# Performance work log

Hardware: AMD Instinct MI355X
Metric: run time of the kernel (lower is better)

## Reference

```python
import jax, jax.numpy as jnp
import numpy as np

S1, S2 = 1024, 1024
DA, DV, DOUT = 2, 64, 1
K1, K2 = 32, 32


def _gelu(x):
    # torch nn.GELU() default is the exact erf-based gelu
    return jax.nn.gelu(x, approximate=False)


def _flayer(Rr, Ri, w, x):
    f = jnp.fft.rfftn(x, axes=(0, 1))[:K1, :K2]            # [K1,K2,DV] complex
    Rf = jnp.einsum('abc,abcd->abd', f, Rr + 1j * Ri)       # [K1,K2,DV] complex
    kernelpart = jnp.fft.irfftn(Rf, s=(S1, S2), axes=(0, 1))  # [S1,S2,DV] real
    return _gelu(kernelpart + x @ w)


def setup_inputs() -> dict:
    key = jax.random.key(0)
    ks = jax.random.split(key, 20)
    d = {}
    d['input'] = jax.random.normal(ks[0], (S1, S2, DA), dtype=jnp.float32)
    d['Wsh'] = jax.random.normal(ks[1], (DA, DV), dtype=jnp.float32) * (1.0 / np.sqrt(DA))
    d['bsh'] = jax.random.normal(ks[2], (DV,), dtype=jnp.float32) * 0.02
    for i, base in zip(range(1, 5), range(3, 15, 3)):
        d[f'Rr{i}'] = jax.random.normal(ks[base], (K1, K2, DV, DV), dtype=jnp.float32) * (1.0 / DV)
        d[f'Ri{i}'] = jax.random.normal(ks[base + 1], (K1, K2, DV, DV), dtype=jnp.float32) * (1.0 / DV)
        d[f'w{i}'] = jax.random.normal(ks[base + 2], (DV, DV), dtype=jnp.float32) * (1.0 / np.sqrt(DV))
    d['Wp'] = jax.random.normal(ks[15], (DV, DOUT), dtype=jnp.float32) * (1.0 / np.sqrt(DV))
    d['bp'] = jax.random.normal(ks[16], (DOUT,), dtype=jnp.float32) * 0.02
    return d


def reference(input, Wsh, bsh, Rr1, Ri1, w1, Rr2, Ri2, w2,
              Rr3, Ri3, w3, Rr4, Ri4, w4, Wp, bp):
    vt = _gelu(input @ Wsh + bsh)          # Shallow: Linear + GELU
    vt = _flayer(Rr1, Ri1, w1, vt)
    vt = _flayer(Rr2, Ri2, w2, vt)
    vt = _flayer(Rr3, Ri3, w3, vt)
    vt = _flayer(Rr4, Ri4, w4, vt)
    u = (vt @ Wp + bp)[:, :, 0]            # Project, take channel 0 -> [S1,S2]
    return u
```

## Files before the change

kernel.cpp:

```cpp
#include <hip/hip_runtime.h>
#include <math.h>

#define MASKN 1023

typedef unsigned short ushort_t;
typedef __attribute__((ext_vector_type(8))) short short8;
typedef __attribute__((ext_vector_type(4))) float floatx4;
typedef __attribute__((ext_vector_type(4))) unsigned short us4v;

__device__ __forceinline__ float gelu_f(float x) {
    float x2 = x * x;
    float inner = fmaf(0.044715f * x, x2, x);
    float t = exp2f(inner * -2.302089214f);
    return x * __builtin_amdgcn_rcpf(1.0f + t);
}

__device__ __forceinline__ float bf2f(ushort_t h) {
    return __uint_as_float(((unsigned int)h) << 16);
}
__device__ __forceinline__ ushort_t f2bf(float f) {
    unsigned int u = __float_as_uint(f);
    u += 0x7FFFu + ((u >> 16) & 1u);
    return (ushort_t)(u >> 16);
}
struct us4 { ushort_t x, y, z, w; };

__device__ __forceinline__ unsigned int pk2bf(float lo, float hi) {
    unsigned int r;
    asm("v_cvt_pk_bf16_f32 %0, %1, %2" : "=v"(r) : "v"(lo), "v"(hi));
    return r;
}

__device__ __forceinline__ void st4(ushort_t* p, float4 v) {
    uint2 w;
    w.x = pk2bf(v.x, v.y);
    w.y = pk2bf(v.z, v.w);
    *(uint2*)p = w;
}

__device__ __forceinline__ void async16(ushort_t* l, const ushort_t* g) {
    __builtin_amdgcn_global_load_lds(
        (const __attribute__((address_space(1))) void*)g,
        (__attribute__((address_space(3))) void*)l, 16, 0, 0);
}

__global__ void k_fill_tw(float* __restrict__ ct, float* __restrict__ st) {
    int j = blockIdx.x * 256 + threadIdx.x;
    float ang = (float)j * (6.283185307179586f / 1024.0f);
    float s, c;
    sincosf(ang, &s, &c);
    ct[j] = c; st[j] = s;
}

__global__ void k_fill_T1(ushort_t* __restrict__ T1h, ushort_t* __restrict__ T1l) {
    int idx = blockIdx.x * 256 + threadIdx.x;
    int k2p = idx >> 10, y = idx & 1023;
    int k2 = k2p >> 1;
    float ang = (float)((k2 * y) & MASKN) * (6.283185307179586f / 1024.0f);
    float s, c;
    sincosf(ang, &s, &c);
    float v = (k2p & 1) ? -s : c;
    ushort_t h = f2bf(v);
    T1h[idx] = h;
    T1l[idx] = f2bf(v - bf2f(h));
}

__global__ void k_fill_T2(ushort_t* __restrict__ T2h, ushort_t* __restrict__ T2l) {
    int idx = blockIdx.x * 256 + threadIdx.x;
    int n2 = idx >> 6, kk = idx & 63;
    int k2 = kk >> 1;
    float ang = (float)((k2 * n2) & MASKN) * (6.283185307179586f / 1024.0f);
    float s, c;
    sincosf(ang, &s, &c);
    float v = (kk & 1) ? -s : c;
    ushort_t h = f2bf(v);
    T2h[idx] = h;
    T2l[idx] = f2bf(v - bf2f(h));
}

__global__ void k_fill_wT(const float* __restrict__ w1, const float* __restrict__ w2,
        const float* __restrict__ w3, const float* __restrict__ w4,
        ushort_t* __restrict__ wTh, ushort_t* __restrict__ wTl) {
    int l = blockIdx.y;
    int i = blockIdx.x * 256 + threadIdx.x;
    int d = i >> 6, c = i & 63;
    const float* w = (l == 0) ? w1 : (l == 1) ? w2 : (l == 2) ? w3 : w4;
    float v = w[c * 64 + d];
    ushort_t h = f2bf(v);
    wTh[l * 4096 + i] = h;
    wTl[l * 4096 + i] = f2bf(v - bf2f(h));
}

__global__ __launch_bounds__(256) void k_shallow(const float* __restrict__ in,
        const float* __restrict__ Wsh, const float* __restrict__ bsh,
        ushort_t* __restrict__ vt) {
    int tid = blockIdx.x * 256 + threadIdx.x;
    int p = tid >> 4, c0 = (tid & 15) << 2;
    float a0 = in[p * 2], a1 = in[p * 2 + 1];
    float4 w0 = *(const float4*)&Wsh[c0];
    float4 w1 = *(const float4*)&Wsh[64 + c0];
    float4 b  = *(const float4*)&bsh[c0];
    float4 r;
    r.x = gelu_f(fmaf(a0, w0.x, fmaf(a1, w1.x, b.x)));
    r.y = gelu_f(fmaf(a0, w0.y, fmaf(a1, w1.y, b.y)));
    r.z = gelu_f(fmaf(a0, w0.z, fmaf(a1, w1.z, b.z)));
    r.w = gelu_f(fmaf(a0, w0.w, fmaf(a1, w1.w, b.w)));
    st4(&vt[(size_t)p * 64 + c0], r);
}

#define VS1 72
__global__ __launch_bounds__(256, 3) void k_f1(const ushort_t* __restrict__ vt,
        const ushort_t* __restrict__ T1h, const ushort_t* __restrict__ T1l,
        float* __restrict__ gT) {
    __shared__ __align__(16) ushort_t t1s[2][8192];
    __shared__ __align__(16) ushort_t vs[2][64 * VS1];
    int t = threadIdx.x;
    int x0 = blockIdx.x * 2;
    int wv = t >> 6, lane = t & 63;
    int lm = lane & 15, quad = lane >> 4;
    int lrow = t & 63, cq = (t >> 6) * 16;
    const ushort_t* vrow0 = vt + (size_t)x0 * 65536;
    const ushort_t* vrow1 = vrow0 + 65536;

    floatx4 acc[2][4];
    #pragma unroll
    for (int xi = 0; xi < 2; ++xi)
        #pragma unroll
        for (int nt = 0; nt < 4; ++nt) acc[xi][nt] = (floatx4)(0.f);

    uint4 pf[2][2][2];
    #pragma unroll
    for (int i = 0; i < 4; ++i) {
        int j = (wv * 4 + i) * 64 + lane;
        int jj = j & 511;
        int r = jj >> 3, du = jj & 7, su = du ^ (r & 7);
        const ushort_t* src = ((j < 512) ? T1h : T1l) + (size_t)r * 1024 + su * 8;
        async16(&t1s[0][(wv * 4 + i) * 512], src);
    }
    __builtin_amdgcn_sched_barrier(0);
    {
        const ushort_t* s00 = vrow0 + (size_t)lrow * 64 + cq;
        pf[0][0][0] = *(const uint4*)(s00);
        pf[0][0][1] = *(const uint4*)(s00 + 8);
        const ushort_t* s01 = vrow1 + (size_t)lrow * 64 + cq;
        pf[0][1][0] = *(const uint4*)(s01);
        pf[0][1][1] = *(const uint4*)(s01 + 8);
        const ushort_t* s10 = vrow0 + (size_t)(64 + lrow) * 64 + cq;
        pf[1][0][0] = *(const uint4*)(s10);
        pf[1][0][1] = *(const uint4*)(s10 + 8);
        const ushort_t* s11 = vrow1 + (size_t)(64 + lrow) * 64 + cq;
        pf[1][1][0] = *(const uint4*)(s11);
        pf[1][1][1] = *(const uint4*)(s11 + 8);
    }
    __builtin_amdgcn_sched_barrier(0);

    for (int hc = 0; hc < 16; ++hc) {
        int b = hc & 1;
        #pragma unroll
        for (int xi = 0; xi < 2; ++xi)
            #pragma unroll
            for (int i = 0; i < 2; ++i) {
                union { uint4 u; ushort_t e[8]; } uv;
                uv.u = pf[b][xi][i];
                #pragma unroll
                for (int j = 0; j < 8; ++j)
                    vs[xi][(cq + i * 8 + j) * VS1 + lrow] = uv.e[j];
            }
        __builtin_amdgcn_sched_barrier(0);
        if (hc < 15) asm volatile("s_waitcnt vmcnt(4)" ::: "memory");
        else         asm volatile("s_waitcnt vmcnt(0)" ::: "memory");
        __builtin_amdgcn_sched_barrier(0);
        __builtin_amdgcn_s_barrier();
        if (hc < 15) {
            #pragma unroll
            for (int i = 0; i < 4; ++i) {
                int j = (wv * 4 + i) * 64 + lane;
                int jj = j & 511;
                int r = jj >> 3, du = jj & 7, su = du ^ (r & 7);
                const ushort_t* src = ((j < 512) ? T1h : T1l)
                                      + (size_t)r * 1024 + (hc + 1) * 64 + su * 8;
                async16(&t1s[b ^ 1][(wv * 4 + i) * 512], src);
            }
        }
        if (hc < 14) {
            const ushort_t* s0 = vrow0 + (size_t)((hc + 2) * 64 + lrow) * 64 + cq;
            pf[b][0][0] = *(const uint4*)(s0);
            pf[b][0][1] = *(const uint4*)(s0 + 8);
            const ushort_t* s1 = vrow1 + (size_t)((hc + 2) * 64 + lrow) * 64 + cq;
            pf[b][1][0] = *(const uint4*)(s1);
            pf[b][1][1] = *(const uint4*)(s1 + 8);
        }
        __builtin_amdgcn_sched_barrier(0);

        #pragma unroll
        for (int ys = 0; ys < 2; ++ys) {
            short8 af0 = *(const short8*)&vs[0][(wv * 16 + lm) * VS1 + ys * 32 + quad * 8];
            short8 af1 = *(const short8*)&vs[1][(wv * 16 + lm) * VS1 + ys * 32 + quad * 8];
            #pragma unroll
            for (int nt = 0; nt < 4; ++nt) {
                int sl = (((ys * 4 + quad) ^ (lm & 7)) * 8);
                short8 bh = *(const short8*)&t1s[b][(nt * 16 + lm) * 64 + sl];
                short8 bl = *(const short8*)&t1s[b][4096 + (nt * 16 + lm) * 64 + sl];
                acc[0][nt] = __builtin_amdgcn_mfma_f32_16x16x32_bf16(af0, bh, acc[0][nt], 0, 0, 0);
                acc[0][nt] = __builtin_amdgcn_mfma_f32_16x16x32_bf16(af0, bl, acc[0][nt], 0, 0, 0);
                acc[1][nt] = __builtin_amdgcn_mfma_f32_16x16x32_bf16(af1, bh, acc[1][nt], 0, 0, 0);
                acc[1][nt] = __builtin_amdgcn_mfma_f32_16x16x32_bf16(af1, bl, acc[1][nt], 0, 0, 0);
            }
        }
    }
    #pragma unroll
    for (int xi = 0; xi < 2; ++xi) {
        float* grow = gT + (size_t)(x0 + xi) * 4096;
        #pragma unroll
        for (int nt = 0; nt < 4; ++nt)
            #pragma unroll
            for (int r = 0; r < 4; ++r)
                grow[(wv * 16 + quad * 4 + r) * 64 + nt * 16 + lm] = acc[xi][nt][r];
    }
}

__global__ __launch_bounds__(256) void k_f2(const float* __restrict__ gT,
        const float* __restrict__ ct, const float* __restrict__ st,
        float* __restrict__ fpr, float* __restrict__ fpi) {
    int t = threadIdx.x;
    int cx = blockIdx.x;
    int cg = blockIdx.y;
    int k10 = blockIdx.z * 8;
    int l = t & 63;
    int q = t >> 6;
    int c = cg * 4 + q;
    int e = l & 1;
    int k2 = l >> 1;
    float acc[8];
    #pragma unroll
    for (int i = 0; i < 8; ++i) acc[i] = 0.f;
    for (int xi = 0; xi < 128; ++xi) {
        int x = cx * 128 + xi;
        float v = gT[(size_t)x * 4096 + c * 64 + l];
        float p = __shfl_xor(v, 1);
        float gr = e ? p : v;
        float gi = e ? v : p;
        float u  = e ? gi : gr;
        float w2 = e ? -gr : gi;
        float cb = ct[x], sb = st[x];
        int ph = (x * k10) & MASKN;
        float cr = ct[ph], sr = st[ph];
        #pragma unroll
        for (int j = 0; j < 8; ++j) {
            acc[j] = fmaf(u, cr, fmaf(w2, sr, acc[j]));
            float nc = fmaf(cr, cb, -sr * sb);
            float ns = fmaf(sr, cb, cr * sb);
            cr = nc; sr = ns;
        }
    }
    float* dst = e ? fpi : fpr;
    #pragma unroll
    for (int j = 0; j < 8; ++j)
        dst[(size_t)cx * 65536 + ((k10 + j) * 32 + k2) * 64 + c] = acc[j];
}

__global__ __launch_bounds__(64) void k_mix(const float* __restrict__ fpr, const float* __restrict__ fpi,
        const float* __restrict__ Rr, const float* __restrict__ Ri,
        float* __restrict__ Rfr, float* __restrict__ Rfi) {
    __shared__ float fr[64], fi[64];
    int m = blockIdx.x;
    int d = threadIdx.x;
    float sr = 0.f, si = 0.f;
    #pragma unroll
    for (int ch = 0; ch < 8; ++ch) {
        sr += fpr[(size_t)ch * 65536 + m * 64 + d];
        si += fpi[(size_t)ch * 65536 + m * 64 + d];
    }
    fr[d] = sr; fi[d] = si;
    __syncthreads();
    const float* Rrb = Rr + (size_t)m * 4096;
    const float* Rib = Ri + (size_t)m * 4096;
    float ar = 0.f, ai = 0.f;
    for (int c = 0; c < 64; ++c) {
        float rr = Rrb[c * 64 + d], ri = Rib[c * 64 + d];
        ar = fmaf(fr[c], rr, fmaf(-fi[c], ri, ar));
        ai = fmaf(fr[c], ri, fmaf(fi[c], rr, ai));
    }
    Rfr[m * 64 + d] = ar;
    Rfi[m * 64 + d] = ai;
}

__global__ __launch_bounds__(256) void k_i1(const float* __restrict__ Rfr, const float* __restrict__ Rfi,
        const float* __restrict__ ctg, const float* __restrict__ stg,
        ushort_t* __restrict__ Bhl) {
    __shared__ float ct[1024], st[1024];
    int t = threadIdx.x;
    #pragma unroll
    for (int i = 0; i < 4; ++i) { int j = t + 256 * i; ct[j] = ctg[j]; st[j] = stg[j]; }
    __syncthreads();
    int n1 = blockIdx.x;
    int d = t & 63;
    int k20 = (t >> 6) * 8;
    float br[8], bi[8];
    #pragma unroll
    for (int j = 0; j < 8; ++j) { br[j] = 0.f; bi[j] = 0.f; }
    int idx = 0;
    for (int k1 = 0; k1 < 32; ++k1) {
        float cc = ct[idx], ss = st[idx];
        idx = (idx + n1) & MASKN;
        #pragma unroll
        for (int j = 0; j < 8; ++j) {
            float rr = Rfr[(k1 * 32 + k20 + j) * 64 + d];
            float ri = Rfi[(k1 * 32 + k20 + j) * 64 + d];
            br[j] = fmaf(rr, cc, fmaf(-ri, ss, br[j]));
            bi[j] = fmaf(rr, ss, fmaf(ri, cc, bi[j]));
        }
    }
    union { uint4 u[2]; ushort_t e[16]; } hh, ll;
    #pragma unroll
    for (int j = 0; j < 8; ++j) {
        int k2 = k20 + j;
        float sc = (k2 == 0 ? 1.0f : 2.0f) * 9.5367431640625e-7f;
        float vr = br[j] * sc, vi = bi[j] * sc;
        ushort_t hr = f2bf(vr), hi2 = f2bf(vi);
        hh.e[2 * j] = hr;          hh.e[2 * j + 1] = hi2;
        ll.e[2 * j] = f2bf(vr - bf2f(hr));
        ll.e[2 * j + 1] = f2bf(vi - bf2f(hi2));
    }
    size_t base = (size_t)n1 * 8192 + d * 64 + 2 * k20;
    *(uint4*)(Bhl + base) = hh.u[0];
    *(uint4*)(Bhl + base + 8) = hh.u[1];
    *(uint4*)(Bhl + 4096 + base) = ll.u[0];
    *(uint4*)(Bhl + 4096 + base + 8) = ll.u[1];
}

__global__ __launch_bounds__(256, 2) void k_i2f(ushort_t* __restrict__ vt,
        ushort_t* Bhl,
        const ushort_t* __restrict__ T2h, const ushort_t* __restrict__ T2l,
        const ushort_t* __restrict__ wTh, const ushort_t* __restrict__ wTl,
        const ushort_t* __restrict__ T1h, const ushort_t* __restrict__ T1l,
        float* gT) {
    __shared__ __align__(16) ushort_t ab[16384];
    __shared__ __align__(16) ushort_t t1s[8192];
    __shared__ __align__(16) ushort_t trans[64 * VS1];
    int t = threadIdx.x;
    int wv = t >> 6, lane = t & 63;
    int lm = lane & 15, quad = lane >> 4;
    int n1 = blockIdx.x;
    const ushort_t* Bhr = Bhl + (size_t)n1 * 8192;
    const ushort_t* Blr = Bhr + 4096;

    {
        const ushort_t* s = (wv == 0) ? Bhr : (wv == 1) ? Blr : (wv == 2) ? wTh : wTl;
        #pragma unroll
        for (int i = 0; i < 8; ++i) {
            int j = i * 64 + lane;
            int r = j >> 3, u = (j & 7) ^ (r & 7);
            async16(&ab[wv * 4096 + i * 512], s + r * 64 + u * 8);
        }
    }

    int n2b = wv * 16 + lm;
    const ushort_t* t2hp = T2h + n2b * 64 + quad * 8;
    const ushort_t* t2lp = T2l + n2b * 64 + quad * 8;
    const ushort_t* vrd  = vt + ((size_t)n1 * 1024 + n2b) * 64 + quad * 8;
    ushort_t*       vst  = vt + ((size_t)n1 * 1024 + n2b) * 64;

    short8 th[2][2], tl[2][2], vv[2][2];
    #pragma unroll
    for (int ks = 0; ks < 2; ++ks) {
        th[0][ks] = *(const short8*)(t2hp + ks * 32);
        tl[0][ks] = *(const short8*)(t2lp + ks * 32);
        vv[0][ks] = *(const short8*)(vrd + ks * 32);
    }
    floatx4 facc[4];
    #pragma unroll
    for (int nt = 0; nt < 4; ++nt) facc[nt] = (floatx4)(0.f);
    __syncthreads();

    int r7 = lm & 7;
    #pragma unroll
    for (int c = 0; c < 16; ++c) {
        #pragma unroll
        for (int i = 0; i < 4; ++i) {
            int j = (wv * 4 + i) * 64 + lane;
            int jj = j & 511;
            int rr_ = jj >> 3, du = jj & 7, su = du ^ (rr_ & 7);
            const ushort_t* src = ((j < 512) ? T1h : T1l)
                                  + (size_t)rr_ * 1024 + c * 64 + su * 8;
            async16(&t1s[(wv * 4 + i) * 512], src);
        }
        __builtin_amdgcn_sched_barrier(0);
        if (c < 15) {
            #pragma unroll
            for (int ks = 0; ks < 2; ++ks) {
                th[(c + 1) & 1][ks] = *(const short8*)(t2hp + (c + 1) * 4096 + ks * 32);
                tl[(c + 1) & 1][ks] = *(const short8*)(t2lp + (c + 1) * 4096 + ks * 32);
                vv[(c + 1) & 1][ks] = *(const short8*)(vrd + (size_t)(c + 1) * 4096 + ks * 32);
            }
        }
        __builtin_amdgcn_sched_barrier(0);

        floatx4 acc[4];
        #pragma unroll
        for (int mt = 0; mt < 4; ++mt) acc[mt] = (floatx4)(0.f);
        __builtin_amdgcn_s_setprio(1);
        #pragma unroll
        for (int ks = 0; ks < 2; ++ks) {
            int sl = ((ks * 4 + quad) ^ r7) * 8;
            #pragma unroll
            for (int mt = 0; mt < 4; ++mt) {
                int ro = (mt * 16 + lm) * 64 + sl;
                short8 ah = *(const short8*)&ab[ro];
                short8 al = *(const short8*)&ab[4096 + ro];
                short8 wh = *(const short8*)&ab[8192 + ro];
                short8 wl = *(const short8*)&ab[12288 + ro];
                acc[mt] = __builtin_amdgcn_mfma_f32_16x16x32_bf16(ah, th[c & 1][ks], acc[mt], 0, 0, 0);
                acc[mt] = __builtin_amdgcn_mfma_f32_16x16x32_bf16(al, th[c & 1][ks], acc[mt], 0, 0, 0);
                acc[mt] = __builtin_amdgcn_mfma_f32_16x16x32_bf16(ah, tl[c & 1][ks], acc[mt], 0, 0, 0);
                acc[mt] = __builtin_amdgcn_mfma_f32_16x16x32_bf16(wh, vv[c & 1][ks], acc[mt], 0, 0, 0);
                acc[mt] = __builtin_amdgcn_mfma_f32_16x16x32_bf16(wl, vv[c & 1][ks], acc[mt], 0, 0, 0);
            }
        }
        __builtin_amdgcn_s_setprio(0);

        uint2 w[4];
        #pragma unroll
        for (int mt = 0; mt < 4; ++mt) {
            w[mt].x = pk2bf(gelu_f(acc[mt][0]), gelu_f(acc[mt][1]));
            w[mt].y = pk2bf(gelu_f(acc[mt][2]), gelu_f(acc[mt][3]));
            *(uint2*)(vst + (size_t)c * 4096 + mt * 16 + quad * 4) = w[mt];
        }
        #pragma unroll
        for (int mt = 0; mt < 4; ++mt) {
            int chb = mt * 16 + quad * 4;
            trans[(chb + 0) * VS1 + n2b] = (ushort_t)(w[mt].x & 0xffffu);
            trans[(chb + 1) * VS1 + n2b] = (ushort_t)(w[mt].x >> 16);
            trans[(chb + 2) * VS1 + n2b] = (ushort_t)(w[mt].y & 0xffffu);
            trans[(chb + 3) * VS1 + n2b] = (ushort_t)(w[mt].y >> 16);
        }
        __builtin_amdgcn_sched_barrier(0);
        asm volatile("s_waitcnt lgkmcnt(0)" ::: "memory");
        if (c < 15) asm volatile("s_waitcnt vmcnt(10)" ::: "memory");
        else        asm volatile("s_waitcnt vmcnt(4)" ::: "memory");
        __builtin_amdgcn_sched_barrier(0);
        __builtin_amdgcn_s_barrier();
        __builtin_amdgcn_sched_barrier(0);

        #pragma unroll
        for (int ys = 0; ys < 2; ++ys) {
            short8 af = *(const short8*)&trans[(wv * 16 + lm) * VS1 + ys * 32 + quad * 8];
            #pragma unroll
            for (int nt = 0; nt < 4; ++nt) {
                int sl = ((ys * 4 + quad) ^ r7) * 8;
                short8 bh = *(const short8*)&t1s[(nt * 16 + lm) * 64 + sl];
                short8 bl = *(const short8*)&t1s[4096 + (nt * 16 + lm) * 64 + sl];
                facc[nt] = __builtin_amdgcn_mfma_f32_16x16x32_bf16(af, bh, facc[nt], 0, 0, 0);
                facc[nt] = __builtin_amdgcn_mfma_f32_16x16x32_bf16(af, bl, facc[nt], 0, 0, 0);
            }
        }
        __builtin_amdgcn_sched_barrier(0);
        __builtin_amdgcn_s_barrier();
        __builtin_amdgcn_sched_barrier(0);
    }

    float* grow = gT + (size_t)n1 * 4096;
    #pragma unroll
    for (int nt = 0; nt < 4; ++nt)
        #pragma unroll
        for (int r = 0; r < 4; ++r)
            grow[(wv * 16 + quad * 4 + r) * 64 + nt * 16 + lm] = facc[nt][r];
}

__global__ __launch_bounds__(256, 4) void k_i2fin(ushort_t* __restrict__ vt,
        const ushort_t* __restrict__ Bhl,
        const ushort_t* __restrict__ T2h, const ushort_t* __restrict__ T2l,
        const ushort_t* __restrict__ wTh, const ushort_t* __restrict__ wTl,
        const float* __restrict__ Wp, const float* __restrict__ bp,
        float* __restrict__ out) {
    __shared__ __align__(16) ushort_t ab[16384];
    int t = threadIdx.x;
    int wv = t >> 6, lane = t & 63;
    int lm = lane & 15, quad = lane >> 4;
    int n1 = blockIdx.x;
    const ushort_t* Bhr = Bhl + (size_t)n1 * 8192;
    const ushort_t* Blr = Bhr + 4096;
    {
        const ushort_t* s = (wv == 0) ? Bhr : (wv == 1) ? Blr : (wv == 2) ? wTh : wTl;
        #pragma unroll
        for (int i = 0; i < 8; ++i) {
            int j = i * 64 + lane;
            int r = j >> 3, u = (j & 7) ^ (r & 7);
            async16(&ab[wv * 4096 + i * 512], s + r * 64 + u * 8);
        }
    }
    int n2b = wv * 16 + lm;
    const ushort_t* t2hp = T2h + n2b * 64 + quad * 8;
    const ushort_t* t2lp = T2l + n2b * 64 + quad * 8;
    const ushort_t* vrd  = vt + ((size_t)n1 * 1024 + n2b) * 64 + quad * 8;
    short8 th[2][2], tl[2][2], vv[2][2];
    #pragma unroll
    for (int ks = 0; ks < 2; ++ks) {
        th[0][ks] = *(const short8*)(t2hp + ks * 32);
        tl[0][ks] = *(const short8*)(t2lp + ks * 32);
        vv[0][ks] = *(const short8*)(vrd + ks * 32);
    }
    float4 wpv[4];
    float bp0 = bp[0];
    #pragma unroll
    for (int mt = 0; mt < 4; ++mt) wpv[mt] = *(const float4*)&Wp[mt * 16 + quad * 4];
    __syncthreads();

    int r7 = lm & 7;
    #pragma unroll
    for (int c = 0; c < 16; ++c) {
        if (c < 15) {
            #pragma unroll
            for (int ks = 0; ks < 2; ++ks) {
                th[(c + 1) & 1][ks] = *(const short8*)(t2hp + (c + 1) * 4096 + ks * 32);
                tl[(c + 1) & 1][ks] = *(const short8*)(t2lp + (c + 1) * 4096 + ks * 32);
                vv[(c + 1) & 1][ks] = *(const short8*)(vrd + (size_t)(c + 1) * 4096 + ks * 32);
            }
        }
        __builtin_amdgcn_sched_barrier(0);
        floatx4 acc[4];
        #pragma unroll
        for (int mt = 0; mt < 4; ++mt) acc[mt] = (floatx4)(0.f);
        __builtin_amdgcn_s_setprio(1);
        #pragma unroll
        for (int ks = 0; ks < 2; ++ks) {
            int sl = ((ks * 4 + quad) ^ r7) * 8;
            #pragma unroll
            for (int mt = 0; mt < 4; ++mt) {
                int ro = (mt * 16 + lm) * 64 + sl;
                short8 ah = *(const short8*)&ab[ro];
                short8 al = *(const short8*)&ab[4096 + ro];
                short8 wh = *(const short8*)&ab[8192 + ro];
                short8 wl = *(const short8*)&ab[12288 + ro];
                acc[mt] = __builtin_amdgcn_mfma_f32_16x16x32_bf16(ah, th[c & 1][ks], acc[mt], 0, 0, 0);
                acc[mt] = __builtin_amdgcn_mfma_f32_16x16x32_bf16(al, th[c & 1][ks], acc[mt], 0, 0, 0);
                acc[mt] = __builtin_amdgcn_mfma_f32_16x16x32_bf16(ah, tl[c & 1][ks], acc[mt], 0, 0, 0);
                acc[mt] = __builtin_amdgcn_mfma_f32_16x16x32_bf16(wh, vv[c & 1][ks], acc[mt], 0, 0, 0);
                acc[mt] = __builtin_amdgcn_mfma_f32_16x16x32_bf16(wl, vv[c & 1][ks], acc[mt], 0, 0, 0);
            }
        }
        __builtin_amdgcn_s_setprio(0);
        float s = 0.f;
        #pragma unroll
        for (int mt = 0; mt < 4; ++mt) {
            s = fmaf(gelu_f(acc[mt][0]), wpv[mt].x, s);
            s = fmaf(gelu_f(acc[mt][1]), wpv[mt].y, s);
            s = fmaf(gelu_f(acc[mt][2]), wpv[mt].z, s);
            s = fmaf(gelu_f(acc[mt][3]), wpv[mt].w, s);
        }
        s += __shfl_xor(s, 16);
        s += __shfl_xor(s, 32);
        if (quad == 0)
            out[(size_t)n1 * 1024 + c * 64 + n2b] = s + bp0;
    }
}

extern "C" void kernel_launch(void* const* d_in, const int* in_sizes, int n_in,
                              void* d_out, int out_size, void* d_ws, size_t ws_size,
                              hipStream_t stream) {
    const float* in  = (const float*)d_in[0];
    const float* Wsh = (const float*)d_in[1];
    const float* bsh = (const float*)d_in[2];
    const float* Wp  = (const float*)d_in[15];
    const float* bp  = (const float*)d_in[16];

    char* wsb = (char*)d_ws;
    ushort_t* vt   = (ushort_t*)wsb;
    float* ctab = (float*)(wsb + 134217728);
    float* stab = ctab + 1024;
    float* gT   = stab + 1024;
    float* Rfr  = gT + 4194304;
    float* Rfi  = Rfr + 65536;
    ushort_t* T1h = (ushort_t*)(Rfi + 65536);
    ushort_t* T1l = T1h + 65536;
    ushort_t* T2h = T1l + 65536;
    ushort_t* T2l = T2h + 65536;
    ushort_t* wTh = T2l + 65536;
    ushort_t* wTl = wTh + 16384;
    ushort_t* Bhl = (ushort_t*)gT;
    float* fpr = (float*)d_out;
    float* fpi = fpr + 524288;

    k_fill_tw<<<4, 256, 0, stream>>>(ctab, stab);
    k_fill_T1<<<256, 256, 0, stream>>>(T1h, T1l);
    k_fill_T2<<<256, 256, 0, stream>>>(T2h, T2l);
    k_fill_wT<<<dim3(16, 4), 256, 0, stream>>>((const float*)d_in[5], (const float*)d_in[8],
                                               (const float*)d_in[11], (const float*)d_in[14], wTh, wTl);
    k_shallow<<<65536, 256, 0, stream>>>(in, Wsh, bsh, vt);
    k_f1<<<512, 256, 0, stream>>>(vt, T1h, T1l, gT);
    for (int L = 0; L < 4; ++L) {
        const float* Rr = (const float*)d_in[3 + L * 3];
        const float* Ri = (const float*)d_in[4 + L * 3];
        k_f2<<<dim3(8, 16, 4), 256, 0, stream>>>(gT, ctab, stab, fpr, fpi);
        k_mix<<<1024, 64, 0, stream>>>(fpr, fpi, Rr, Ri, Rfr, Rfi);
        k_i1<<<1024, 256, 0, stream>>>(Rfr, Rfi, ctab, stab, Bhl);
        if (L < 3) {
            k_i2f<<<1024, 256, 0, stream>>>(vt, Bhl, T2h, T2l,
                    wTh + L * 4096, wTl + L * 4096, T1h, T1l, gT);
        } else {
            k_i2fin<<<1024, 256, 0, stream>>>(vt, Bhl, T2h, T2l,
                    wTh + L * 4096, wTl + L * 4096, Wp, bp, (float*)d_out);
        }
    }
}
```

Baseline: 713.2 us.

## Double-buffer T1 tile and transpose buffer in k_i2f, drop trailing barrier

```diff
diff --git a/kernel.cpp b/kernel.cpp
--- a/kernel.cpp
+++ b/kernel.cpp
@@ -336,8 +336,8 @@
         const ushort_t* __restrict__ T1h, const ushort_t* __restrict__ T1l,
         float* gT) {
     __shared__ __align__(16) ushort_t ab[16384];
-    __shared__ __align__(16) ushort_t t1s[8192];
-    __shared__ __align__(16) ushort_t trans[64 * VS1];
+    __shared__ __align__(16) ushort_t t1s[2][8192];
+    __shared__ __align__(16) ushort_t trans[2][4096];
     int t = threadIdx.x;
     int wv = t >> 6, lane = t & 63;
     int lm = lane & 15, quad = lane >> 4;
@@ -354,6 +354,14 @@
             async16(&ab[wv * 4096 + i * 512], s + r * 64 + u * 8);
         }
     }
+    #pragma unroll
+    for (int i = 0; i < 4; ++i) {
+        int j = (wv * 4 + i) * 64 + lane;
+        int jj = j & 511;
+        int rr_ = jj >> 3, du = jj & 7, su = du ^ (rr_ & 7);
+        const ushort_t* src = ((j < 512) ? T1h : T1l) + (size_t)rr_ * 1024 + su * 8;
+        async16(&t1s[0][(wv * 4 + i) * 512], src);
+    }
 
     int n2b = wv * 16 + lm;
     const ushort_t* t2hp = T2h + n2b * 64 + quad * 8;
@@ -374,24 +382,16 @@
     __syncthreads();
 
     int r7 = lm & 7;
+    int u3 = n2b >> 3, e3 = n2b & 7;
     #pragma unroll
     for (int c = 0; c < 16; ++c) {
-        #pragma unroll
-        for (int i = 0; i < 4; ++i) {
-            int j = (wv * 4 + i) * 64 + lane;
-            int jj = j & 511;
-            int rr_ = jj >> 3, du = jj & 7, su = du ^ (rr_ & 7);
-            const ushort_t* src = ((j < 512) ? T1h : T1l)
-                                  + (size_t)rr_ * 1024 + c * 64 + su * 8;
-            async16(&t1s[(wv * 4 + i) * 512], src);
-        }
-        __builtin_amdgcn_sched_barrier(0);
-        if (c < 15) {
+        int b = c & 1;
+        {
             #pragma unroll
             for (int ks = 0; ks < 2; ++ks) {
-                th[(c + 1) & 1][ks] = *(const short8*)(t2hp + (c + 1) * 4096 + ks * 32);
-                tl[(c + 1) & 1][ks] = *(const short8*)(t2lp + (c + 1) * 4096 + ks * 32);
-                vv[(c + 1) & 1][ks] = *(const short8*)(vrd + (size_t)(c + 1) * 4096 + ks * 32);
+                th[b ^ 1][ks] = *(const short8*)(t2hp + (c + 1) * 4096 + ks * 32);
+                tl[b ^ 1][ks] = *(const short8*)(t2lp + (c + 1) * 4096 + ks * 32);
+                vv[b ^ 1][ks] = *(const short8*)(vrd + (size_t)(c + 1) * 4096 + ks * 32);
             }
         }
         __builtin_amdgcn_sched_barrier(0);
@@ -410,11 +410,11 @@
                 short8 al = *(const short8*)&ab[4096 + ro];
                 short8 wh = *(const short8*)&ab[8192 + ro];
                 short8 wl = *(const short8*)&ab[12288 + ro];
-                acc[mt] = __builtin_amdgcn_mfma_f32_16x16x32_bf16(ah, th[c & 1][ks], acc[mt], 0, 0, 0);
-                acc[mt] = __builtin_amdgcn_mfma_f32_16x16x32_bf16(al, th[c & 1][ks], acc[mt], 0, 0, 0);
-                acc[mt] = __builtin_amdgcn_mfma_f32_16x16x32_bf16(ah, tl[c & 1][ks], acc[mt], 0, 0, 0);
-                acc[mt] = __builtin_amdgcn_mfma_f32_16x16x32_bf16(wh, vv[c & 1][ks], acc[mt], 0, 0, 0);
-                acc[mt] = __builtin_amdgcn_mfma_f32_16x16x32_bf16(wl, vv[c & 1][ks], acc[mt], 0, 0, 0);
+                acc[mt] = __builtin_amdgcn_mfma_f32_16x16x32_bf16(ah, th[b][ks], acc[mt], 0, 0, 0);
+                acc[mt] = __builtin_amdgcn_mfma_f32_16x16x32_bf16(al, th[b][ks], acc[mt], 0, 0, 0);
+                acc[mt] = __builtin_amdgcn_mfma_f32_16x16x32_bf16(ah, tl[b][ks], acc[mt], 0, 0, 0);
+                acc[mt] = __builtin_amdgcn_mfma_f32_16x16x32_bf16(wh, vv[b][ks], acc[mt], 0, 0, 0);
+                acc[mt] = __builtin_amdgcn_mfma_f32_16x16x32_bf16(wl, vv[b][ks], acc[mt], 0, 0, 0);
             }
         }
         __builtin_amdgcn_s_setprio(0);
@@ -426,36 +426,51 @@
             w[mt].y = pk2bf(gelu_f(acc[mt][2]), gelu_f(acc[mt][3]));
             *(uint2*)(vst + (size_t)c * 4096 + mt * 16 + quad * 4) = w[mt];
         }
+        ushort_t* tb = trans[b];
         #pragma unroll
         for (int mt = 0; mt < 4; ++mt) {
             int chb = mt * 16 + quad * 4;
-            trans[(chb + 0) * VS1 + n2b] = (ushort_t)(w[mt].x & 0xffffu);
-            trans[(chb + 1) * VS1 + n2b] = (ushort_t)(w[mt].x >> 16);
-            trans[(chb + 2) * VS1 + n2b] = (ushort_t)(w[mt].y & 0xffffu);
-            trans[(chb + 3) * VS1 + n2b] = (ushort_t)(w[mt].y >> 16);
+            #pragma unroll
+            for (int r = 0; r < 4; ++r) {
+                int ch = chb + r;
+                ushort_t val = (r == 0) ? (ushort_t)(w[mt].x & 0xffffu)
+                             : (r == 1) ? (ushort_t)(w[mt].x >> 16)
+                             : (r == 2) ? (ushort_t)(w[mt].y & 0xffffu)
+                                        : (ushort_t)(w[mt].y >> 16);
+                tb[ch * 64 + ((u3 ^ (ch & 7)) << 3) + e3] = val;
+            }
         }
         __builtin_amdgcn_sched_barrier(0);
         asm volatile("s_waitcnt lgkmcnt(0)" ::: "memory");
-        if (c < 15) asm volatile("s_waitcnt vmcnt(10)" ::: "memory");
-        else        asm volatile("s_waitcnt vmcnt(4)" ::: "memory");
+        asm volatile("s_waitcnt vmcnt(10)" ::: "memory");
         __builtin_amdgcn_sched_barrier(0);
         __builtin_amdgcn_s_barrier();
         __builtin_amdgcn_sched_barrier(0);
 
         #pragma unroll
+        for (int i = 0; i < 4; ++i) {
+            int j = (wv * 4 + i) * 64 + lane;
+            int jj = j & 511;
+            int rr_ = jj >> 3, du = jj & 7, su = du ^ (rr_ & 7);
+            const ushort_t* src = ((j < 512) ? T1h : T1l)
+                                  + (size_t)rr_ * 1024 + (c + 1) * 64 + su * 8;
+            async16(&t1s[b ^ 1][(wv * 4 + i) * 512], src);
+        }
+        __builtin_amdgcn_sched_barrier(0);
+
+        #pragma unroll
         for (int ys = 0; ys < 2; ++ys) {
-            short8 af = *(const short8*)&trans[(wv * 16 + lm) * VS1 + ys * 32 + quad * 8];
+            int ch = wv * 16 + lm;
+            short8 af = *(const short8*)&trans[b][ch * 64 + (((ys * 4 + quad) ^ (ch & 7)) << 3)];
             #pragma unroll
             for (int nt = 0; nt < 4; ++nt) {
                 int sl = ((ys * 4 + quad) ^ r7) * 8;
-                short8 bh = *(const short8*)&t1s[(nt * 16 + lm) * 64 + sl];
-                short8 bl = *(const short8*)&t1s[4096 + (nt * 16 + lm) * 64 + sl];
+                short8 bh = *(const short8*)&t1s[b][(nt * 16 + lm) * 64 + sl];
+                short8 bl = *(const short8*)&t1s[b][4096 + (nt * 16 + lm) * 64 + sl];
                 facc[nt] = __builtin_amdgcn_mfma_f32_16x16x32_bf16(af, bh, facc[nt], 0, 0, 0);
                 facc[nt] = __builtin_amdgcn_mfma_f32_16x16x32_bf16(af, bl, facc[nt], 0, 0, 0);
             }
         }
-        __builtin_amdgcn_sched_barrier(0);
-        __builtin_amdgcn_s_barrier();
         __builtin_amdgcn_sched_barrier(0);
     }
 
```

New measurement: 716.7 us. About the same (+0.5%).
